# Kernel tuning notes

Measured on AMD Instinct MI355X. Metric: run time of the kernel, lower is better.

The kernel has to match this reference:

```python
import jax, jax.numpy as jnp
import numpy as np

DIM = 64   # flow dimension
HID = 8    # hidden_dim=[8]
B = 131072 # batch of samples


def setup_inputs() -> dict:
    key = jax.random.key(0)
    ks = jax.random.split(key, 6)
    L = DIM - 1  # number of per-dim MLPs (layers[0..L-1], layer l has fan-in l+1)
    lim = float(np.sqrt(0.5))
    x = jax.random.normal(ks[0], (B, DIM), jnp.float32)
    initial_param = jax.random.uniform(ks[1], (2,), jnp.float32, -lim, lim)
    # Ragged Linear(fan_in=l+1, 8) weights stacked into padded [L, HID, L];
    # entries beyond column l are masked to zero in reference().
    fan_in = np.arange(1, DIM).astype(np.float32)          # (L,)
    bnd1 = (1.0 / np.sqrt(fan_in))[:, None, None]          # torch Linear default init bound
    W1 = jax.random.uniform(ks[2], (L, HID, L), jnp.float32, -1.0, 1.0) * bnd1
    b1 = jax.random.uniform(ks[3], (L, HID), jnp.float32, -1.0, 1.0) * bnd1[:, :, 0]
    bnd2 = 1.0 / np.sqrt(HID)
    W2 = jax.random.uniform(ks[4], (L, 2, HID), jnp.float32, -bnd2, bnd2)
    b2 = jax.random.uniform(ks[5], (L, 2), jnp.float32, -bnd2, bnd2)
    return {"x": x, "initial_param": initial_param, "W1": W1, "b1": b1, "W2": W2, "b2": b2}


def reference(x, initial_param, W1, b1, W2, b2):
    B_, D = x.shape
    L = W1.shape[0]  # D - 1
    # mask[l, d] = 1 iff d <= l  ->  layer l sees exactly x[:, :l+1]
    mask = jnp.tril(jnp.ones((L, L), x.dtype))
    W1m = W1 * mask[:, None, :]
    # all dim-1 tiny MLPs fused into two batched contractions
    h = jnp.tanh(jnp.einsum('bd,lhd->blh', x[:, :L], W1m) + b1)   # [B, L, HID]
    out = jnp.einsum('blh,loh->blo', h, W2) + b2                   # [B, L, 2]
    mu0 = jnp.broadcast_to(initial_param[0], (B_, 1)).astype(x.dtype)
    al0 = jnp.broadcast_to(initial_param[1], (B_, 1)).astype(x.dtype)
    mu = jnp.concatenate([mu0, out[:, :, 0]], axis=1)              # [B, D]
    alpha = jnp.concatenate([al0, out[:, :, 1]], axis=1)           # [B, D]
    z = x * jnp.exp(alpha) + mu
    log_det = jnp.sum(alpha, axis=1)
    return z, log_det
```

## Files before the change

### kernel.cpp

```cpp
#include <hip/hip_runtime.h>


#define DIMS 64
#define TPB  512
#define WAVES 8
#define SPW  16

typedef __attribute__((ext_vector_type(8))) short short8;
typedef __attribute__((ext_vector_type(4))) float f32x4;
typedef __attribute__((ext_vector_type(4))) unsigned int uint4v;
typedef unsigned short ushort_t;
typedef unsigned int uint_t;

#if __has_builtin(__builtin_amdgcn_exp2f)
#define YSCALE 2.8853900817779268f
#define EXPY(x) __builtin_amdgcn_exp2f(x)
#define EXP2F(x) __builtin_amdgcn_exp2f(x)
#else
#define YSCALE 2.0f
#define EXPY(x) __expf(x)
#define EXP2F(x) exp2f(x)
#endif
#define LOG2E 1.4426950408889634f

#define A_OFF 0
#define BLO_OFF 16384
#define BHI_OFF 32768
#define C_OFF 49152
#define WT_BYTES 55808
#define CDE_BYTES 6656
#define PREP_N (24576 + 1664)

#define XZ_OFF CDE_BYTES
#define LDS_BYTES (CDE_BYTES + WAVES * SPW * DIMS * 4)

__device__ __align__(16) unsigned char g_ws[WT_BYTES];

__device__ __forceinline__ uint_t pk2bf(float a, float b) {
#if __has_builtin(__builtin_amdgcn_cvt_pk_bf16_f32)
    typedef __attribute__((ext_vector_type(2))) __bf16 bf16x2;
    bf16x2 r = __builtin_amdgcn_cvt_pk_bf16_f32(a, b);
    return __builtin_bit_cast(uint_t, r);
#else
    uint_t ua = __float_as_uint(a); ua += 0x7FFFu + ((ua >> 16) & 1u);
    uint_t ub = __float_as_uint(b); ub += 0x7FFFu + ((ub >> 16) & 1u);
    return (ub & 0xFFFF0000u) | (ua >> 16);
#endif
}

__device__ __forceinline__ ushort_t f2bf(float f) {
    uint_t u = __float_as_uint(f);
    u += 0x7FFFu + ((u >> 16) & 1u);
    return (ushort_t)(u >> 16);
}

__device__ __forceinline__ int logrow(int p) {
    int n = p & 15;
    return (p >> 5) * 32 + (n >> 2) * 8 + ((p >> 4) & 1) * 4 + (n & 3);
}

__global__ void siaf_prep(const float* __restrict__ W1, const float* __restrict__ b1,
                          const float* __restrict__ W2, const float* __restrict__ b2) {
    ushort_t* __restrict__ ws_u = (ushort_t*)g_ws;
    int i = blockIdx.x * 256 + threadIdx.x;
    if (i < 8192) {
        int p = i >> 5, k = i & 31;
        int L = logrow(p), l = L >> 3, h = L & 7;
        float v = (k <= l) ? W1[(l * 8 + h) * 63 + k] * YSCALE : 0.0f;
        ws_u[i] = f2bf(v);
    } else if (i < 16384) {
        int r = i - 8192;
        int p = 256 + (r >> 5), k = r & 31;
        int L = logrow(p), l = L >> 3, h = L & 7;
        float v = (l < 63 && k <= l) ? W1[(l * 8 + h) * 63 + k] * YSCALE : 0.0f;
        ws_u[i] = f2bf(v);
    } else if (i < 24576) {
        int r = i - 16384;
        int p = 256 + (r >> 5), k = 32 + (r & 31);
        int L = logrow(p), l = L >> 3, h = L & 7;
        float v = (l < 63 && k <= l) ? W1[(l * 8 + h) * 63 + k] * YSCALE : 0.0f;
        ws_u[i] = f2bf(v);
    } else if (i < PREP_N) {
        int f = i - 24576;
        float* fws = (float*)(ws_u + 24576);
        float v = 0.0f;
        if (f < 1024) {
            int l = f >> 4, o = (f >> 3) & 1, h = f & 7;
            if (l < 63) v = W2[(l * 2 + o) * 8 + h];
        } else if (f < 1536) {
            int p = f - 1024;
            int L = logrow(p), l = L >> 3, h = L & 7;
            if (l < 63) v = b1[l * 8 + h] * YSCALE;
        } else {
            int j = f - 1536, l = j >> 1, o = j & 1;
            if (l < 63) v = b2[l * 2 + o];
        }
        fws[f] = v;
    }
}

__device__ __forceinline__ float th(float t) {
    float e = EXPY(t);
    float r = __builtin_amdgcn_rcpf(e + 1.0f);
    return fmaf(-2.0f, r, 1.0f);
}

__global__ __launch_bounds__(TPB, 8) void siaf_main(
        const float* __restrict__ x, const float* __restrict__ ip,
        float* __restrict__ out, int nB) {
    extern __shared__ unsigned char lds[];

    const int tid  = threadIdx.x;
    const int wv   = tid >> 6, lane = tid & 63;
    const int s16  = lane & 15, quad = lane >> 4;
    const int sbase = blockIdx.x * (WAVES * SPW) + wv * SPW;
    float* xzw = (float*)(lds + XZ_OFF) + wv * (SPW * DIMS);

    #pragma unroll
    for (int g = 0; g < 4; ++g) {
        const float4 v = ((const float4*)(x + (size_t)sbase * DIMS))[g * 64 + lane];
        const int s_loc = 4 * g + quad;
        const int pc = (s16 ^ s_loc) & 15;
        *(float4*)(xzw + s_loc * 64 + pc * 4) = v;
    }
    const float ip0 = ip[0], ip1 = ip[1];

    if (tid < CDE_BYTES / 16) {
        ((uint4*)lds)[tid] = ((const uint4*)(g_ws + C_OFF))[tid];
    }

    short8 bfr[2];
    #pragma unroll
    for (int kh = 0; kh < 2; ++kh) {
        const int c0 = kh * 8 + quad * 2;
        float4 va = *(const float4*)(xzw + s16 * 64 + ((c0 ^ s16) & 15) * 4);
        float4 vb = *(const float4*)(xzw + s16 * 64 + (((c0 + 1) ^ s16) & 15) * 4);
        uint4v u = {pk2bf(va.x, va.y), pk2bf(va.z, va.w),
                    pk2bf(vb.x, vb.y), pk2bf(vb.z, vb.w)};
        bfr[kh] = __builtin_bit_cast(short8, u);
    }

    __syncthreads();

    const float* w2f = (const float*)(lds);
    const float* b1f = (const float*)(lds + 4096);
    const float* b2f = (const float*)(lds + 6144);

    const ushort_t* gA   = (const ushort_t*)g_ws;
    const ushort_t* gBlo = (const ushort_t*)(g_ws + BLO_OFF);
    const ushort_t* gBhi = (const ushort_t*)(g_ws + BHI_OFF);
    const int fo = s16 * 32 + quad * 8;

    auto ldA = [&](int w, short8& a00, short8& a10, short8& a01, short8& a11) {
        if (w < 8) {
            const ushort_t* b = gA + w * 1024 + fo;
            a00 = *(const short8*)(b);
            a10 = *(const short8*)(b + 512);
        } else {
            const int off = (w - 8) * 1024 + fo;
            a00 = *(const short8*)(gBlo + off);
            a10 = *(const short8*)(gBlo + off + 512);
            a01 = *(const short8*)(gBhi + off);
            a11 = *(const short8*)(gBhi + off + 512);
        }
    };

    short8 A00[2], A10[2], A01[2] = {}, A11[2] = {};
    ldA(0, A00[0], A10[0], A01[0], A11[0]);

    float lsum = 0.0f;
    #pragma unroll
    for (int w = 0; w < 16; ++w) {
        const int cur = w & 1, nxt = cur ^ 1;

        if (w < 15) ldA(w + 1, A00[nxt], A10[nxt], A01[nxt], A11[nxt]);

        const float4 bi0 = *(const float4*)(b1f + w * 32 + quad * 4);
        const float4 bi1 = *(const float4*)(b1f + w * 32 + 16 + quad * 4);

        f32x4 aE = {bi0.x, bi0.y, bi0.z, bi0.w};
        f32x4 aO = {bi1.x, bi1.y, bi1.z, bi1.w};
        aE = __builtin_amdgcn_mfma_f32_16x16x32_bf16(A00[cur], bfr[0], aE, 0, 0, 0);
        aO = __builtin_amdgcn_mfma_f32_16x16x32_bf16(A10[cur], bfr[0], aO, 0, 0, 0);
        if (w >= 8) {
            aE = __builtin_amdgcn_mfma_f32_16x16x32_bf16(A01[cur], bfr[1], aE, 0, 0, 0);
            aO = __builtin_amdgcn_mfma_f32_16x16x32_bf16(A11[cur], bfr[1], aO, 0, 0, 0);
        }

        const float t0 = th(aE[0]), t1 = th(aE[1]), t2 = th(aE[2]), t3 = th(aE[3]);
        const float t4 = th(aO[0]), t5 = th(aO[1]), t6 = th(aO[2]), t7 = th(aO[3]);

        const int l = 4 * w + quad;
        const float4 m0 = *(const float4*)(w2f + l * 16);
        const float4 m1 = *(const float4*)(w2f + l * 16 + 4);
        const float4 a0 = *(const float4*)(w2f + l * 16 + 8);
        const float4 a1 = *(const float4*)(w2f + l * 16 + 12);
        const float2 bb = *(const float2*)(b2f + l * 2);

        float mu0 = bb.x, mu1 = m1.x * t4;
        mu0 = fmaf(m0.x, t0, mu0); mu1 = fmaf(m1.y, t5, mu1);
        mu0 = fmaf(m0.y, t1, mu0); mu1 = fmaf(m1.z, t6, mu1);
        mu0 = fmaf(m0.z, t2, mu0); mu1 = fmaf(m1.w, t7, mu1);
        mu0 = fmaf(m0.w, t3, mu0);
        const float mu = mu0 + mu1;
        float al0 = bb.y, al1 = a1.x * t4;
        al0 = fmaf(a0.x, t0, al0); al1 = fmaf(a1.y, t5, al1);
        al0 = fmaf(a0.y, t1, al0); al1 = fmaf(a1.z, t6, al1);
        al0 = fmaf(a0.z, t2, al0); al1 = fmaf(a1.w, t7, al1);
        al0 = fmaf(a0.w, t3, al0);
        const float al = al0 + al1;

        const bool pad = (l == 63);
        const float alB = pad ? ip1 : al;
        const float muB = pad ? ip0 : mu;
        const int d = pad ? 0 : (l + 1);
        float* pz = xzw + s16 * 64 + ((((d >> 2) ^ s16) & 15) << 2) + (d & 3);
        *pz = fmaf(*pz, EXP2F(alB * LOG2E), muB);
        lsum += alB;
    }

    #pragma unroll
    for (int g = 0; g < 4; ++g) {
        const int s_loc = 4 * g + quad;
        const int pc = (s16 ^ s_loc) & 15;
        const float4 v = *(const float4*)(xzw + s_loc * 64 + pc * 4);
        ((float4*)(out + (size_t)sbase * DIMS))[g * 64 + lane] = v;
    }

    {
        float v = lsum;
        int r1 = __builtin_amdgcn_ds_swizzle(__float_as_int(v), 0x401F);
        v += __int_as_float(r1);
        int r2 = __builtin_amdgcn_ds_bpermute((lane ^ 32) << 2, __float_as_int(v));
        v += __int_as_float(r2);
        if (quad == 0)
            out[(size_t)nB * DIMS + sbase + s16] = v;
    }
}

extern "C" void kernel_launch(void* const* d_in, const int* in_sizes, int n_in,
                              void* d_out, int out_size, void* d_ws, size_t ws_size,
                              hipStream_t stream) {
    const float* x  = (const float*)d_in[0];
    const float* ip = (const float*)d_in[1];
    const float* W1 = (const float*)d_in[2];
    const float* b1 = (const float*)d_in[3];
    const float* W2 = (const float*)d_in[4];
    const float* b2 = (const float*)d_in[5];
    float* out = (float*)d_out;
    (void)d_ws; (void)ws_size;

    const int nB = in_sizes[0] / DIMS;

    (void)hipFuncSetAttribute((const void*)siaf_main,
                              hipFuncAttributeMaxDynamicSharedMemorySize, LDS_BYTES);

    siaf_prep<<<(PREP_N + 255) / 256, 256, 0, stream>>>(W1, b1, W2, b2);
    siaf_main<<<nB / (WAVES * SPW), TPB, LDS_BYTES, stream>>>(x, ip, out, nB);
}
```

Before: 114.0 us.

## Fuse weight prep into main kernel via cooperative grid sync; sigmoid-form tanh

Merges the weight-packing prep kernel and the main kernel into one cooperative launch: every block stages its x tile, some threads do the prep work, and a grid-wide sync separates the phases. The goal is to remove a second kernel launch and the gap between launches. It also rewrites tanh as a sigmoid by folding the -2 scale, the constant offset and log2e into W2/b2 at prep time, which drops an fma per activation and the per-element alpha*LOG2E multiply. The grid sync requires all 1024 blocks to be resident at once, and the fallback keeps the two-kernel path if the cooperative launch fails.

```diff
diff --git a/kernel.cpp b/kernel.cpp
--- a/kernel.cpp
+++ b/kernel.cpp
@@ -1,10 +1,14 @@
 #include <hip/hip_runtime.h>
-
+#include <hip/hip_cooperative_groups.h>
+
+
+namespace cg = cooperative_groups;
 
 #define DIMS 64
 #define TPB  512
 #define WAVES 8
 #define SPW  16
+#define GRID 1024
 
 typedef __attribute__((ext_vector_type(8))) short short8;
 typedef __attribute__((ext_vector_type(4))) float f32x4;
@@ -14,14 +18,13 @@
 
 #if __has_builtin(__builtin_amdgcn_exp2f)
 #define YSCALE 2.8853900817779268f
-#define EXPY(x) __builtin_amdgcn_exp2f(x)
 #define EXP2F(x) __builtin_amdgcn_exp2f(x)
 #else
-#define YSCALE 2.0f
-#define EXPY(x) __expf(x)
+#define YSCALE 2.8853900817779268f
 #define EXP2F(x) exp2f(x)
 #endif
 #define LOG2E 1.4426950408889634f
+#define LN2   0.6931471805599453f
 
 #define A_OFF 0
 #define BLO_OFF 16384
@@ -59,10 +62,10 @@
     return (p >> 5) * 32 + (n >> 2) * 8 + ((p >> 4) & 1) * 4 + (n & 3);
 }
 
-__global__ void siaf_prep(const float* __restrict__ W1, const float* __restrict__ b1,
-                          const float* __restrict__ W2, const float* __restrict__ b2) {
+__device__ __forceinline__ void prep_element(int i,
+        const float* __restrict__ W1, const float* __restrict__ b1,
+        const float* __restrict__ W2, const float* __restrict__ b2) {
     ushort_t* __restrict__ ws_u = (ushort_t*)g_ws;
-    int i = blockIdx.x * 256 + threadIdx.x;
     if (i < 8192) {
         int p = i >> 5, k = i & 31;
         int L = logrow(p), l = L >> 3, h = L & 7;
@@ -82,40 +85,43 @@
         ws_u[i] = f2bf(v);
     } else if (i < PREP_N) {
         int f = i - 24576;
-        float* fws = (float*)(ws_u + 24576);
+        float* fws = (float*)(g_ws + C_OFF);
         float v = 0.0f;
         if (f < 1024) {
             int l = f >> 4, o = (f >> 3) & 1, h = f & 7;
-            if (l < 63) v = W2[(l * 2 + o) * 8 + h];
+            if (l < 63) {
+                v = -2.0f * W2[(l * 2 + o) * 8 + h];
+                if (o) v *= LOG2E;
+            }
         } else if (f < 1536) {
             int p = f - 1024;
             int L = logrow(p), l = L >> 3, h = L & 7;
             if (l < 63) v = b1[l * 8 + h] * YSCALE;
         } else {
             int j = f - 1536, l = j >> 1, o = j & 1;
-            if (l < 63) v = b2[l * 2 + o];
+            if (l < 63) {
+                float s = b2[l * 2 + o];
+                #pragma unroll
+                for (int h = 0; h < 8; ++h) s += W2[(l * 2 + o) * 8 + h];
+                v = o ? s * LOG2E : s;
+            }
         }
         fws[f] = v;
     }
 }
 
-__device__ __forceinline__ float th(float t) {
-    float e = EXPY(t);
-    float r = __builtin_amdgcn_rcpf(e + 1.0f);
-    return fmaf(-2.0f, r, 1.0f);
-}
-
-__global__ __launch_bounds__(TPB, 8) void siaf_main(
-        const float* __restrict__ x, const float* __restrict__ ip,
-        float* __restrict__ out, int nB) {
-    extern __shared__ unsigned char lds[];
-
-    const int tid  = threadIdx.x;
-    const int wv   = tid >> 6, lane = tid & 63;
-    const int s16  = lane & 15, quad = lane >> 4;
-    const int sbase = blockIdx.x * (WAVES * SPW) + wv * SPW;
-    float* xzw = (float*)(lds + XZ_OFF) + wv * (SPW * DIMS);
-
+__global__ void siaf_prep(const float* __restrict__ W1, const float* __restrict__ b1,
+                          const float* __restrict__ W2, const float* __restrict__ b2) {
+    prep_element(blockIdx.x * 256 + threadIdx.x, W1, b1, W2, b2);
+}
+
+__device__ __forceinline__ float sg(float t) {
+    float e = EXP2F(t);
+    return __builtin_amdgcn_rcpf(e + 1.0f);
+}
+
+__device__ __forceinline__ void x_stage(float* xzw, const float* __restrict__ x,
+                                        int sbase, int s16, int quad, int lane) {
     #pragma unroll
     for (int g = 0; g < 4; ++g) {
         const float4 v = ((const float4*)(x + (size_t)sbase * DIMS))[g * 64 + lane];
@@ -123,7 +129,21 @@
         const int pc = (s16 ^ s_loc) & 15;
         *(float4*)(xzw + s_loc * 64 + pc * 4) = v;
     }
-    const float ip0 = ip[0], ip1 = ip[1];
+}
+
+__device__ __forceinline__ void siaf_body(
+        unsigned char* lds, const float* __restrict__ x,
+        const float* __restrict__ ip, float* __restrict__ out, int nB,
+        bool stage_x) {
+    const int tid  = threadIdx.x;
+    const int wv   = tid >> 6, lane = tid & 63;
+    const int s16  = lane & 15, quad = lane >> 4;
+    const int sbase = blockIdx.x * (WAVES * SPW) + wv * SPW;
+    float* xzw = (float*)(lds + XZ_OFF) + wv * (SPW * DIMS);
+
+    if (stage_x) x_stage(xzw, x, sbase, s16, quad, lane);
+    const float ip0 = ip[0];
+    const float ip1l2 = ip[1] * LOG2E;
 
     if (tid < CDE_BYTES / 16) {
         ((uint4*)lds)[tid] = ((const uint4*)(g_ws + C_OFF))[tid];
@@ -172,7 +192,6 @@
     #pragma unroll
     for (int w = 0; w < 16; ++w) {
         const int cur = w & 1, nxt = cur ^ 1;
-
         if (w < 15) ldA(w + 1, A00[nxt], A10[nxt], A01[nxt], A11[nxt]);
 
         const float4 bi0 = *(const float4*)(b1f + w * 32 + quad * 4);
@@ -187,8 +206,8 @@
             aO = __builtin_amdgcn_mfma_f32_16x16x32_bf16(A11[cur], bfr[1], aO, 0, 0, 0);
         }
 
-        const float t0 = th(aE[0]), t1 = th(aE[1]), t2 = th(aE[2]), t3 = th(aE[3]);
-        const float t4 = th(aO[0]), t5 = th(aO[1]), t6 = th(aO[2]), t7 = th(aO[3]);
+        const float r0 = sg(aE[0]), r1 = sg(aE[1]), r2 = sg(aE[2]), r3 = sg(aE[3]);
+        const float r4 = sg(aO[0]), r5 = sg(aO[1]), r6 = sg(aO[2]), r7 = sg(aO[3]);
 
         const int l = 4 * w + quad;
         const float4 m0 = *(const float4*)(w2f + l * 16);
@@ -197,26 +216,29 @@
         const float4 a1 = *(const float4*)(w2f + l * 16 + 12);
         const float2 bb = *(const float2*)(b2f + l * 2);
 
-        float mu0 = bb.x, mu1 = m1.x * t4;
-        mu0 = fmaf(m0.x, t0, mu0); mu1 = fmaf(m1.y, t5, mu1);
-        mu0 = fmaf(m0.y, t1, mu0); mu1 = fmaf(m1.z, t6, mu1);
-        mu0 = fmaf(m0.z, t2, mu0); mu1 = fmaf(m1.w, t7, mu1);
-        mu0 = fmaf(m0.w, t3, mu0);
-        const float mu = mu0 + mu1;
-        float al0 = bb.y, al1 = a1.x * t4;
-        al0 = fmaf(a0.x, t0, al0); al1 = fmaf(a1.y, t5, al1);
-        al0 = fmaf(a0.y, t1, al0); al1 = fmaf(a1.z, t6, al1);
-        al0 = fmaf(a0.z, t2, al0); al1 = fmaf(a1.w, t7, al1);
-        al0 = fmaf(a0.w, t3, al0);
-        const float al = al0 + al1;
-
-        const bool pad = (l == 63);
-        const float alB = pad ? ip1 : al;
-        const float muB = pad ? ip0 : mu;
-        const int d = pad ? 0 : (l + 1);
+        float mu0 = bb.x, mu1 = m1.x * r4;
+        mu0 = fmaf(m0.x, r0, mu0); mu1 = fmaf(m1.y, r5, mu1);
+        mu0 = fmaf(m0.y, r1, mu0); mu1 = fmaf(m1.z, r6, mu1);
+        mu0 = fmaf(m0.z, r2, mu0); mu1 = fmaf(m1.w, r7, mu1);
+        mu0 = fmaf(m0.w, r3, mu0);
+        float mu = mu0 + mu1;
+        float al0 = bb.y, al1 = a1.x * r4;
+        al0 = fmaf(a0.x, r0, al0); al1 = fmaf(a1.y, r5, al1);
+        al0 = fmaf(a0.y, r1, al0); al1 = fmaf(a1.z, r6, al1);
+        al0 = fmaf(a0.z, r2, al0); al1 = fmaf(a1.w, r7, al1);
+        al0 = fmaf(a0.w, r3, al0);
+        float alg = al0 + al1;
+
+        int d = l + 1;
+        if (w == 15) {
+            const bool pad = (quad == 3);
+            alg = pad ? ip1l2 : alg;
+            mu  = pad ? ip0 : mu;
+            d   = pad ? 0 : d;
+        }
         float* pz = xzw + s16 * 64 + ((((d >> 2) ^ s16) & 15) << 2) + (d & 3);
-        *pz = fmaf(*pz, EXP2F(alB * LOG2E), muB);
-        lsum += alB;
+        *pz = fmaf(*pz, EXP2F(alg), mu);
+        lsum += alg;
     }
 
     #pragma unroll
@@ -234,8 +256,38 @@
         int r2 = __builtin_amdgcn_ds_bpermute((lane ^ 32) << 2, __float_as_int(v));
         v += __int_as_float(r2);
         if (quad == 0)
-            out[(size_t)nB * DIMS + sbase + s16] = v;
-    }
+            out[(size_t)nB * DIMS + sbase + s16] = v * LN2;
+    }
+}
+
+__global__ __launch_bounds__(TPB, 8) void siaf_main_fb(
+        const float* __restrict__ x, const float* __restrict__ ip,
+        float* __restrict__ out, int nB) {
+    extern __shared__ unsigned char lds[];
+    siaf_body(lds, x, ip, out, nB, true);
+}
+
+__global__ __launch_bounds__(TPB, 8) void siaf_fused(
+        const float* __restrict__ x, const float* __restrict__ ip,
+        const float* __restrict__ W1, const float* __restrict__ b1,
+        const float* __restrict__ W2, const float* __restrict__ b2,
+        float* __restrict__ out, int nB) {
+    extern __shared__ unsigned char lds[];
+    const int tid  = threadIdx.x;
+    const int wv   = tid >> 6, lane = tid & 63;
+    const int s16  = lane & 15, quad = lane >> 4;
+    const int sbase = blockIdx.x * (WAVES * SPW) + wv * SPW;
+    float* xzw = (float*)(lds + XZ_OFF) + wv * (SPW * DIMS);
+
+    x_stage(xzw, x, sbase, s16, quad, lane);
+
+    const int gi = blockIdx.x * TPB + tid;
+    if (gi < PREP_N) prep_element(gi, W1, b1, W2, b2);
+
+    __threadfence();
+    cg::this_grid().sync();
+
+    siaf_body(lds, x, ip, out, nB, false);
 }
 
 extern "C" void kernel_launch(void* const* d_in, const int* in_sizes, int n_in,
@@ -251,10 +303,32 @@
     (void)d_ws; (void)ws_size;
 
     const int nB = in_sizes[0] / DIMS;
-
-    (void)hipFuncSetAttribute((const void*)siaf_main,
+    const int grid = nB / (WAVES * SPW);
+
+    (void)hipFuncSetAttribute((const void*)siaf_fused,
                               hipFuncAttributeMaxDynamicSharedMemorySize, LDS_BYTES);
-
-    siaf_prep<<<(PREP_N + 255) / 256, 256, 0, stream>>>(W1, b1, W2, b2);
-    siaf_main<<<nB / (WAVES * SPW), TPB, LDS_BYTES, stream>>>(x, ip, out, nB);
-}
+    (void)hipFuncSetAttribute((const void*)siaf_main_fb,
+                              hipFuncAttributeMaxDynamicSharedMemorySize, LDS_BYTES);
+
+    static int coop_ok = -1;
+    if (coop_ok < 0) {
+        int maxb = 0;
+        hipError_t e = hipOccupancyMaxActiveBlocksPerMultiprocessor(
+            &maxb, (const void*)siaf_fused, TPB, LDS_BYTES);
+        coop_ok = (e == hipSuccess && maxb >= 4) ? 1 : 0;
+    }
+
+    bool launched = false;
+    if (coop_ok == 1) {
+        void* args[] = {(void*)&x, (void*)&ip, (void*)&W1, (void*)&b1,
+                        (void*)&W2, (void*)&b2, (void*)&out, (void*)&nB};
+        hipError_t e = hipLaunchCooperativeKernel(
+            (const void*)siaf_fused, dim3(grid), dim3(TPB), args, LDS_BYTES, stream);
+        if (e == hipSuccess) launched = true;
+        else coop_ok = 0;
+    }
+    if (!launched) {
+        siaf_prep<<<(PREP_N + 255) / 256, 256, 0, stream>>>(W1, b1, W2, b2);
+        siaf_main_fb<<<grid, TPB, LDS_BYTES, stream>>>(x, ip, out, nB);
+    }
+}
```

Result: no change. 113.6 us (-0.3%).
